# Performance work log

Hardware: AMD Instinct MI355X
Metric: run time of the kernel (lower is better)

## Reference

```python
import jax, jax.numpy as jnp
import numpy as np

NUM_EXPERTS = 8
TOP_K = 2
B, L, H = 4, 4096, 1024


def setup_inputs() -> dict:
    key = jax.random.key(0)
    ks = jax.random.split(key, 5)
    s = 1.0 / np.sqrt(H)
    return {
        "hidden_states": jax.random.normal(ks[0], (B, L, H), dtype=jnp.float32),
        "gate_w": jax.random.normal(ks[1], (H, NUM_EXPERTS), dtype=jnp.float32) * s,
        "w1": jax.random.normal(ks[2], (NUM_EXPERTS, H, 2 * H), dtype=jnp.float32) * s,
        "b1": jnp.zeros((NUM_EXPERTS, 2 * H), dtype=jnp.float32),
        "w2": jax.random.normal(ks[3], (NUM_EXPERTS, 2 * H, H), dtype=jnp.float32) * (1.0 / np.sqrt(2 * H)),
        "b2": jnp.zeros((NUM_EXPERTS, H), dtype=jnp.float32),
    }


def reference(hidden_states, gate_w, w1, b1, w2, b2):
    b, l, h = hidden_states.shape
    flat = hidden_states.reshape(-1, h)                      # [T, H]
    router_logits = flat @ gate_w                            # [T, E]
    probs = jax.nn.softmax(router_logits, axis=-1)
    weights, indices = jax.lax.top_k(probs, TOP_K)           # [T, K]
    weights = weights / jnp.sum(weights, axis=-1, keepdims=True)
    # combine[t, e] = sum_k weights[t, k] * 1{indices[t, k] == e}
    onehot = jax.nn.one_hot(indices, NUM_EXPERTS, dtype=flat.dtype)  # [T, K, E]
    combine = jnp.einsum('tk,tke->te', weights, onehot)      # [T, E]
    out = jnp.zeros_like(flat)
    for e in range(NUM_EXPERTS):  # fixed small expert loop; dense-compute, sparse-combine
        hdn = jax.nn.relu(flat @ w1[e] + b1[e])              # [T, 2H]
        y = hdn @ w2[e] + b2[e]                              # [T, H]
        out = out + combine[:, e:e + 1] * y
    return out.reshape(b, l, h)
```

## Files before the change

kernel.cpp:

```cpp
#include <hip/hip_runtime.h>
#include <hip/hip_bf16.h>
#include <stdint.h>

#define T_TOK 16384
#define HD    1024
#define HD2   2048
#define NE    8
#define ROWS  (2*T_TOK)
#define MAXT  264
#define MT256 136
#define RTOK  32

#define M_NT    256
#define M_OFFS  272
#define M_TILES 288

typedef __bf16 bf16x8 __attribute__((ext_vector_type(8)));
typedef float f32x4 __attribute__((ext_vector_type(4)));

#define GLD16(g, l) __builtin_amdgcn_global_load_lds( \
    (const __attribute__((address_space(1))) void*)(g), \
    (__attribute__((address_space(3))) void*)(l), 16, 0, 0)

__device__ inline unsigned short f2bf(float f) {
    unsigned int u = __float_as_uint(f);
    unsigned int r = (u + 0x7fffu + ((u >> 16) & 1u)) >> 16;
    return (unsigned short)r;
}

__global__ __launch_bounds__(256) void cvt_wT(const float* __restrict__ w,
                                              unsigned short* __restrict__ wt,
                                              int K, int N) {
    __shared__ float t[32][33];
    int e = blockIdx.z;
    int n0 = blockIdx.x * 32, k0 = blockIdx.y * 32;
    int r = threadIdx.x >> 3;
    int c4 = (threadIdx.x & 7) * 4;
    const float* src = w + ((size_t)e * K + k0 + r) * N + n0 + c4;
    float4 v = *(const float4*)src;
    t[r][c4] = v.x; t[r][c4+1] = v.y; t[r][c4+2] = v.z; t[r][c4+3] = v.w;
    __syncthreads();
    int cc = threadIdx.x & 7;
    ushort4 o;
    o.x = f2bf(t[cc*4+0][r]); o.y = f2bf(t[cc*4+1][r]);
    o.z = f2bf(t[cc*4+2][r]); o.w = f2bf(t[cc*4+3][r]);
    *(ushort4*)(wt + ((size_t)e * N + n0 + r) * K + k0 + cc*4) = o;
}

__global__ __launch_bounds__(256) void router_k(const float* __restrict__ x,
        const float* __restrict__ gw, int* __restrict__ meta,
        int* __restrict__ tok_e, int* __restrict__ tok_slot, float* __restrict__ tok_w,
        unsigned short* __restrict__ xb) {
    __shared__ float g[NE * HD];
    __shared__ int   le[RTOK * 2];
    __shared__ float lw[RTOK * 2];
    __shared__ int   lslot[RTOK * 2];
    __shared__ int   lcnt[NE];
    __shared__ int   lbase[NE];
    for (int i = threadIdx.x; i < NE * HD; i += 256) {
        int k = i >> 3, e = i & 7;
        g[e * HD + k] = gw[i];
    }
    if (threadIdx.x < NE) lcnt[threadIdx.x] = 0;
    __syncthreads();

    int wave = threadIdx.x >> 6, lane = threadIdx.x & 63;
    int t0 = blockIdx.x * RTOK;
    for (int i = 0; i < RTOK / 4; i++) {
        int tt = wave * (RTOK / 4) + i;
        int t = t0 + tt;
        const float4* xr = (const float4*)(x + (size_t)t * HD);
        float acc[NE];
#pragma unroll
        for (int e = 0; e < NE; e++) acc[e] = 0.f;
#pragma unroll
        for (int j = 0; j < HD / 256; j++) {
            float4 xv = xr[lane + 64 * j];
            ushort4 o4;
            o4.x = f2bf(xv.x); o4.y = f2bf(xv.y);
            o4.z = f2bf(xv.z); o4.w = f2bf(xv.w);
            *(ushort4*)(xb + (size_t)t * HD + (lane + 64 * j) * 4) = o4;
#pragma unroll
            for (int e = 0; e < NE; e++) {
                float4 gv = *(const float4*)&g[e * HD + (lane + 64 * j) * 4];
                acc[e] += xv.x * gv.x + xv.y * gv.y + xv.z * gv.z + xv.w * gv.w;
            }
        }
#pragma unroll
        for (int e = 0; e < NE; e++) {
            float v = acc[e];
#pragma unroll
            for (int off = 32; off > 0; off >>= 1) v += __shfl_down(v, off, 64);
            acc[e] = v;
        }
        if (lane == 0) {
            int e1 = 0; float l1 = acc[0];
#pragma unroll
            for (int e = 1; e < NE; e++) if (acc[e] > l1) { l1 = acc[e]; e1 = e; }
            int e2 = -1; float l2 = -3.0e38f;
#pragma unroll
            for (int e = 0; e < NE; e++) if (e != e1 && acc[e] > l2) { l2 = acc[e]; e2 = e; }
            float w1 = 1.f / (1.f + expf(l2 - l1));
            le[tt * 2] = e1;     le[tt * 2 + 1] = e2;
            lw[tt * 2] = w1;     lw[tt * 2 + 1] = 1.f - w1;
        }
    }
    __syncthreads();
    if (threadIdx.x < RTOK * 2)
        lslot[threadIdx.x] = atomicAdd(&lcnt[le[threadIdx.x]], 1);
    __syncthreads();
    if (threadIdx.x < NE)
        lbase[threadIdx.x] = atomicAdd(&meta[threadIdx.x * 32], lcnt[threadIdx.x]);
    __syncthreads();
    if (threadIdx.x < RTOK * 2) {
        int gi = t0 * 2 + threadIdx.x;
        int e = le[threadIdx.x];
        tok_e[gi]    = e;
        tok_slot[gi] = lbase[e] + lslot[threadIdx.x];
        tok_w[gi]    = lw[threadIdx.x];
    }
}

__global__ __launch_bounds__(64) void offsets_k(int* __restrict__ meta) {
    int lane = threadIdx.x;
    int cl = (lane < NE) ? meta[lane * 32] : 0;
    int cnt[NE], offs[NE], tbase[NE];
    int o = 0, tb = 0;
#pragma unroll
    for (int e = 0; e < NE; e++) {
        cnt[e] = __shfl(cl, e, 64);
        offs[e] = o;  o += cnt[e];
        tbase[e] = tb; tb += (cnt[e] + 255) >> 8;
    }
    int nt = tb;
    if (lane == 0) meta[M_NT] = nt;
    if (lane < NE) meta[M_OFFS + lane] = offs[lane];
    for (int i = lane; i < nt; i += 64) {
        int e = 0;
#pragma unroll
        for (int k = 1; k < NE; k++) if (i >= tbase[k]) e = k;
        int m = i - tbase[e];
        int r0 = offs[e] + m * 256;
        int re = offs[e] + cnt[e];
        if (r0 + 256 < re) re = r0 + 256;
        meta[M_TILES + i] = e;
        meta[M_TILES + MAXT + i] = r0;
        meta[M_TILES + 2 * MAXT + i] = re;
    }
}

__global__ __launch_bounds__(256) void scatter_k(const int* __restrict__ meta,
        const int* __restrict__ tok_e, const int* __restrict__ tok_slot,
        const float* __restrict__ tok_w, int* __restrict__ rows_tok,
        float* __restrict__ rows_w) {
    int i = blockIdx.x * 256 + threadIdx.x;
    const int* offs = meta + M_OFFS;
    int e = tok_e[i];
    int r = offs[e] + tok_slot[i];
    rows_tok[r] = i >> 1;
    rows_w[r] = tok_w[i];
}


#define ST_A(H, SB, KTN) do { \
    GLD16(pa[H][0] + (KTN) * 64, &As[(SB) + ((H) * 1024 + w * 64) * 8]); \
    GLD16(pa[H][1] + (KTN) * 64, &As[(SB) + ((H) * 1024 + 512 + w * 64) * 8]); } while (0)
#define ST_B(H, SB, KTN) do { \
    GLD16(pb[H][0] + (KTN) * 64, &Bs[(SB) + ((H) * 1024 + w * 64) * 8]); \
    GLD16(pb[H][1] + (KTN) * 64, &Bs[(SB) + ((H) * 1024 + 512 + w * 64) * 8]); } while (0)
#define LD_A(AH, RBUF) do { \
    _Pragma("unroll") \
    for (int im_ = 0; im_ < 4; im_++) { \
        int row_ = (AH) * 128 + wm * 64 + im_ * 16 + rl; \
        _Pragma("unroll") \
        for (int ks_ = 0; ks_ < 2; ks_++) { \
            int g_ = (ks_ * 4 + q) ^ (row_ & 7); \
            af[im_][ks_] = *(const bf16x8*)&As[(RBUF) + row_ * 64 + g_ * 8]; \
        } } } while (0)
#define LD_B(DST, BH, RBUF) do { \
    _Pragma("unroll") \
    for (int in_ = 0; in_ < 2; in_++) { \
        int row_ = (BH) * 128 + wn * 32 + in_ * 16 + rl; \
        _Pragma("unroll") \
        for (int ks_ = 0; ks_ < 2; ks_++) { \
            int g_ = (ks_ * 4 + q) ^ (row_ & 7); \
            DST[in_][ks_] = *(const bf16x8*)&Bs[(RBUF) + row_ * 64 + g_ * 8]; \
        } } } while (0)
#define MM(AH, BH, BF) do { \
    _Pragma("unroll") \
    for (int im_ = 0; im_ < 4; im_++) \
    _Pragma("unroll") \
    for (int in_ = 0; in_ < 2; in_++) \
    _Pragma("unroll") \
    for (int ks_ = 0; ks_ < 2; ks_++) \
        acc[AH][BH][im_][in_] = __builtin_amdgcn_mfma_f32_16x16x32_bf16( \
            af[im_][ks_], BF[in_][ks_], acc[AH][BH][im_][in_], 0, 0, 0); } while (0)
#define SB0()  __builtin_amdgcn_sched_barrier(0)
#define VMW4() do { asm volatile("s_waitcnt vmcnt(4)" ::: "memory"); SB0(); } while (0)
#define BAR()  do { __builtin_amdgcn_s_barrier(); SB0(); } while (0)
#define PRIO(P) __builtin_amdgcn_s_setprio(P)

__global__ __launch_bounds__(512, 2) void gemm1_k(
    const unsigned short* __restrict__ Xbf,
    const unsigned short* __restrict__ W1T,
    const float* __restrict__ b1,
    const int* __restrict__ meta,
    const int* __restrict__ rows_tok,
    unsigned short* __restrict__ hdn)
{
    __shared__ unsigned short As[2 * 16384];
    __shared__ unsigned short Bs[2 * 16384];
    int nt = meta[M_NT];
    int fid = blockIdx.y * 8 + blockIdx.x;
    int lid = (fid & 7) * MT256 + (fid >> 3);
    int xx = lid & 7, mt = lid >> 3;
    if (mt >= nt) return;
    int e    = meta[M_TILES + mt];
    int r0   = meta[M_TILES + MAXT + mt];
    int rend = meta[M_TILES + 2 * MAXT + mt];
    int n0 = xx * 256;

    int tid = threadIdx.x, w = tid >> 6, lane = tid & 63;
    int wm = w >> 2, wn = w & 3;
    int rl = lane & 15, q = lane >> 4;

    const unsigned short* pa[2][2];
    const unsigned short* pb[2][2];
#pragma unroll
    for (int h = 0; h < 2; h++)
#pragma unroll
        for (int c = 0; c < 2; c++) {
            int gg = c * 512 + tid;
            int row = gg >> 3, cc = gg & 7, cl = cc ^ (row & 7);
            int grow = r0 + h * 128 + row;
            grow = grow < ROWS - 1 ? grow : ROWS - 1;
            int tok = rows_tok[grow];
            pa[h][c] = Xbf + (size_t)tok * HD + cl * 8;
            pb[h][c] = W1T + ((size_t)e * HD2 + n0 + h * 128 + row) * HD + cl * 8;
        }

    f32x4 acc[2][2][4][2];
#pragma unroll
    for (int a = 0; a < 2; a++)
#pragma unroll
    for (int b = 0; b < 2; b++)
#pragma unroll
    for (int i = 0; i < 4; i++)
#pragma unroll
    for (int n = 0; n < 2; n++)
        acc[a][b][i][n] = (f32x4){0.f, 0.f, 0.f, 0.f};

    bf16x8 af[4][2], bf0[2][2], bf1[2][2];

    ST_A(0, 0, 0); ST_B(0, 0, 0); ST_B(1, 0, 0); ST_A(1, 0, 0);
    VMW4(); BAR();

#pragma unroll 1
    for (int kt = 0; kt < HD / 64; kt++) {
        int rbuf = (kt & 1) << 14;
        int sbuf = rbuf ^ 16384;
        int ktn = (kt + 1 < HD / 64) ? kt + 1 : HD / 64 - 1;
        LD_A(0, rbuf); LD_B(bf0, 0, rbuf);
        ST_A(0, sbuf, ktn);
        VMW4(); BAR();
        PRIO(1); MM(0, 0, bf0); PRIO(0);
        BAR();
        LD_B(bf1, 1, rbuf);
        ST_B(0, sbuf, ktn);
        VMW4(); BAR();
        PRIO(1); MM(0, 1, bf1); PRIO(0);
        BAR();
        LD_A(1, rbuf);
        ST_B(1, sbuf, ktn);
        BAR();
        PRIO(1); MM(1, 1, bf1); PRIO(0);
        BAR();
        LD_B(bf0, 0, rbuf);
        ST_A(1, sbuf, ktn);
        VMW4(); BAR();
        PRIO(1); MM(1, 0, bf0); PRIO(0);
        BAR();
    }

    const float* b1e = b1 + (size_t)e * HD2;
#pragma unroll
    for (int ah = 0; ah < 2; ah++)
#pragma unroll
    for (int bh = 0; bh < 2; bh++)
#pragma unroll
    for (int in = 0; in < 2; in++) {
        int col = n0 + bh * 128 + wn * 32 + in * 16 + rl;
        float bias = b1e[col];
#pragma unroll
        for (int im = 0; im < 4; im++) {
            int rb2 = r0 + ah * 128 + wm * 64 + im * 16 + q * 4;
#pragma unroll
            for (int j = 0; j < 4; j++) {
                int r = rb2 + j;
                if (r < rend) {
                    float v = acc[ah][bh][im][in][j] + bias;
                    v = v > 0.f ? v : 0.f;
                    hdn[(size_t)r * HD2 + col] = f2bf(v);
                }
            }
        }
    }
}

__global__ __launch_bounds__(512, 2) void gemm2_k(
    const unsigned short* __restrict__ hdn,
    const unsigned short* __restrict__ W2T,
    const float* __restrict__ b2,
    const int* __restrict__ meta,
    const int* __restrict__ rows_tok,
    const float* __restrict__ rows_w,
    float* __restrict__ out)
{
    __shared__ unsigned short As[2 * 16384];
    __shared__ unsigned short Bs[2 * 16384];
    int nt = meta[M_NT];
    int fid = blockIdx.y * 4 + blockIdx.x;
    int lid = (fid & 7) * (MT256 / 2) + (fid >> 3);
    int xx = lid & 3, mt = lid >> 2;
    if (mt >= nt) return;
    int e    = meta[M_TILES + mt];
    int r0   = meta[M_TILES + MAXT + mt];
    int rend = meta[M_TILES + 2 * MAXT + mt];
    int n0 = xx * 256;

    int tid = threadIdx.x, w = tid >> 6, lane = tid & 63;
    int wm = w >> 2, wn = w & 3;
    int rl = lane & 15, q = lane >> 4;

    const unsigned short* pa[2][2];
    const unsigned short* pb[2][2];
#pragma unroll
    for (int h = 0; h < 2; h++)
#pragma unroll
        for (int c = 0; c < 2; c++) {
            int gg = c * 512 + tid;
            int row = gg >> 3, cc = gg & 7, cl = cc ^ (row & 7);
            int grow = r0 + h * 128 + row;
            grow = grow < ROWS - 1 ? grow : ROWS - 1;
            pa[h][c] = hdn + (size_t)grow * HD2 + cl * 8;
            pb[h][c] = W2T + ((size_t)e * HD + n0 + h * 128 + row) * HD2 + cl * 8;
        }

    f32x4 acc[2][2][4][2];
#pragma unroll
    for (int a = 0; a < 2; a++)
#pragma unroll
    for (int b = 0; b < 2; b++)
#pragma unroll
    for (int i = 0; i < 4; i++)
#pragma unroll
    for (int n = 0; n < 2; n++)
        acc[a][b][i][n] = (f32x4){0.f, 0.f, 0.f, 0.f};

    bf16x8 af[4][2], bf0[2][2], bf1[2][2];

    ST_A(0, 0, 0); ST_B(0, 0, 0); ST_B(1, 0, 0); ST_A(1, 0, 0);
    VMW4(); BAR();

#pragma unroll 1
    for (int kt = 0; kt < HD2 / 64; kt++) {
        int rbuf = (kt & 1) << 14;
        int sbuf = rbuf ^ 16384;
        int ktn = (kt + 1 < HD2 / 64) ? kt + 1 : HD2 / 64 - 1;
        LD_A(0, rbuf); LD_B(bf0, 0, rbuf);
        ST_A(0, sbuf, ktn);
        VMW4(); BAR();
        PRIO(1); MM(0, 0, bf0); PRIO(0);
        BAR();
        LD_B(bf1, 1, rbuf);
        ST_B(0, sbuf, ktn);
        VMW4(); BAR();
        PRIO(1); MM(0, 1, bf1); PRIO(0);
        BAR();
        LD_A(1, rbuf);
        ST_B(1, sbuf, ktn);
        BAR();
        PRIO(1); MM(1, 1, bf1); PRIO(0);
        BAR();
        LD_B(bf0, 0, rbuf);
        ST_A(1, sbuf, ktn);
        VMW4(); BAR();
        PRIO(1); MM(1, 0, bf0); PRIO(0);
        BAR();
    }

    const float* b2e = b2 + (size_t)e * HD;
    float bias[2][2];
#pragma unroll
    for (int bh = 0; bh < 2; bh++)
#pragma unroll
        for (int in = 0; in < 2; in++)
            bias[bh][in] = b2e[n0 + bh * 128 + wn * 32 + in * 16 + rl];
#pragma unroll
    for (int ah = 0; ah < 2; ah++)
#pragma unroll
    for (int im = 0; im < 4; im++) {
        int rb2 = r0 + ah * 128 + wm * 64 + im * 16 + q * 4;
#pragma unroll
        for (int j = 0; j < 4; j++) {
            int r = rb2 + j;
            if (r < rend) {
                int tok = rows_tok[r];
                float wt = rows_w[r];
                float* op = out + (size_t)tok * HD + n0;
#pragma unroll
                for (int bh = 0; bh < 2; bh++)
#pragma unroll
                for (int in = 0; in < 2; in++) {
                    float v = (acc[ah][bh][im][in][j] + bias[bh][in]) * wt;
                    atomicAdd(op + bh * 128 + wn * 32 + in * 16 + rl, v);
                }
            }
        }
    }
}

extern "C" void kernel_launch(void* const* d_in, const int* in_sizes, int n_in,
                              void* d_out, int out_size, void* d_ws, size_t ws_size,
                              hipStream_t stream) {
    const float* x  = (const float*)d_in[0];
    const float* gw = (const float*)d_in[1];
    const float* w1 = (const float*)d_in[2];
    const float* b1 = (const float*)d_in[3];
    const float* w2 = (const float*)d_in[4];
    const float* b2 = (const float*)d_in[5];
    float* out = (float*)d_out;

    uint8_t* ws = (uint8_t*)d_ws;
    unsigned short* Xbf = (unsigned short*)(ws);
    unsigned short* W1T = (unsigned short*)(ws + 33554432ull);
    unsigned short* W2T = (unsigned short*)(ws + 67108864ull);
    unsigned short* HDN = (unsigned short*)(ws + 100663296ull);
    int*   meta     = (int*)(ws + 234881024ull);
    int*   tok_e    = meta + 2048;
    int*   tok_slot = tok_e + ROWS;
    float* tok_w    = (float*)(tok_slot + ROWS);
    int*   rows_tok = (int*)(tok_w + ROWS);
    float* rows_w   = (float*)(rows_tok + ROWS);

    hipMemsetAsync(meta, 0, 1024, stream);
    hipMemsetAsync(d_out, 0, (size_t)out_size * sizeof(float), stream);

    cvt_wT<<<dim3(HD2 / 32, HD / 32, NE), 256, 0, stream>>>(w1, W1T, HD, HD2);
    cvt_wT<<<dim3(HD / 32, HD2 / 32, NE), 256, 0, stream>>>(w2, W2T, HD2, HD);
    router_k<<<T_TOK / RTOK, 256, 0, stream>>>(x, gw, meta, tok_e, tok_slot, tok_w, Xbf);
    offsets_k<<<1, 64, 0, stream>>>(meta);
    scatter_k<<<ROWS / 256, 256, 0, stream>>>(meta, tok_e, tok_slot, tok_w, rows_tok, rows_w);
    gemm1_k<<<dim3(HD2 / 256, MT256), 512, 0, stream>>>(Xbf, W1T, b1, meta, rows_tok, HDN);
    gemm2_k<<<dim3(HD / 256, MT256), 512, 0, stream>>>(HDN, W2T, b2, meta, rows_tok, rows_w, out);
}
```

Before: 794.7 us.

## Replace double-buffered K=64 pipeline with 4-stage K=32 async load ring

Both expert GEMM kernels switch from a two-buffer K=64 tile loop, with four barrier-separated quarter-MMA phases and priority toggles, to a four-slot ring of K=32 tiles. Loads are issued three steps ahead and waited on with vmcnt(12). Each K step loads B fragments once and runs all A halves against them, with a new XOR swizzle for 32-wide LDS rows. The intent is deeper memory latency hiding and fewer barriers per unit of MFMA work. In exchange there are twice as many outer iterations with two barriers each, and the smaller K chunk per step may reduce load efficiency.

After: 756.5 us. 1.05x faster.

```diff
diff --git a/kernel.cpp b/kernel.cpp
--- a/kernel.cpp
+++ b/kernel.cpp
@@ -162,43 +162,45 @@
 }
 
 
-#define ST_A(H, SB, KTN) do { \
-    GLD16(pa[H][0] + (KTN) * 64, &As[(SB) + ((H) * 1024 + w * 64) * 8]); \
-    GLD16(pa[H][1] + (KTN) * 64, &As[(SB) + ((H) * 1024 + 512 + w * 64) * 8]); } while (0)
-#define ST_B(H, SB, KTN) do { \
-    GLD16(pb[H][0] + (KTN) * 64, &Bs[(SB) + ((H) * 1024 + w * 64) * 8]); \
-    GLD16(pb[H][1] + (KTN) * 64, &Bs[(SB) + ((H) * 1024 + 512 + w * 64) * 8]); } while (0)
-#define LD_A(AH, RBUF) do { \
+#define ISSUE(KK, NT_) do { \
+    int kk_ = (KK) < (NT_) ? (KK) : (NT_) - 1; \
+    int bb_ = ((KK) & 3) * 8192; \
+    GLD16(pa0 + kk_ * 32, &As[bb_ + (w * 64) * 8]); \
+    GLD16(pa1 + kk_ * 32, &As[bb_ + (512 + w * 64) * 8]); \
+    GLD16(pb0 + kk_ * 32, &Bs[bb_ + (w * 64) * 8]); \
+    GLD16(pb1 + kk_ * 32, &Bs[bb_ + (512 + w * 64) * 8]); } while (0)
+#define SB0()   __builtin_amdgcn_sched_barrier(0)
+#define VMW12() do { asm volatile("s_waitcnt vmcnt(12)" ::: "memory"); SB0(); } while (0)
+#define VMW0()  do { asm volatile("s_waitcnt vmcnt(0)" ::: "memory"); SB0(); } while (0)
+#define BAR()   do { __builtin_amdgcn_s_barrier(); SB0(); } while (0)
+
+#define KSTEP(RB) do { \
+    bf16x8 af[4], bfr[2][2]; \
     _Pragma("unroll") \
-    for (int im_ = 0; im_ < 4; im_++) { \
-        int row_ = (AH) * 128 + wm * 64 + im_ * 16 + rl; \
-        _Pragma("unroll") \
-        for (int ks_ = 0; ks_ < 2; ks_++) { \
-            int g_ = (ks_ * 4 + q) ^ (row_ & 7); \
-            af[im_][ks_] = *(const bf16x8*)&As[(RBUF) + row_ * 64 + g_ * 8]; \
-        } } } while (0)
-#define LD_B(DST, BH, RBUF) do { \
+    for (int bh_ = 0; bh_ < 2; bh_++) \
     _Pragma("unroll") \
     for (int in_ = 0; in_ < 2; in_++) { \
-        int row_ = (BH) * 128 + wn * 32 + in_ * 16 + rl; \
+        int row_ = bh_ * 128 + wn * 32 + in_ * 16 + rl; \
+        int ph_ = q ^ ((row_ >> 1) & 3); \
+        bfr[bh_][in_] = *(const bf16x8*)&Bs[(RB) + row_ * 32 + ph_ * 8]; \
+    } \
+    _Pragma("unroll") \
+    for (int ah_ = 0; ah_ < 2; ah_++) { \
         _Pragma("unroll") \
-        for (int ks_ = 0; ks_ < 2; ks_++) { \
-            int g_ = (ks_ * 4 + q) ^ (row_ & 7); \
-            DST[in_][ks_] = *(const bf16x8*)&Bs[(RBUF) + row_ * 64 + g_ * 8]; \
-        } } } while (0)
-#define MM(AH, BH, BF) do { \
-    _Pragma("unroll") \
-    for (int im_ = 0; im_ < 4; im_++) \
-    _Pragma("unroll") \
-    for (int in_ = 0; in_ < 2; in_++) \
-    _Pragma("unroll") \
-    for (int ks_ = 0; ks_ < 2; ks_++) \
-        acc[AH][BH][im_][in_] = __builtin_amdgcn_mfma_f32_16x16x32_bf16( \
-            af[im_][ks_], BF[in_][ks_], acc[AH][BH][im_][in_], 0, 0, 0); } while (0)
-#define SB0()  __builtin_amdgcn_sched_barrier(0)
-#define VMW4() do { asm volatile("s_waitcnt vmcnt(4)" ::: "memory"); SB0(); } while (0)
-#define BAR()  do { __builtin_amdgcn_s_barrier(); SB0(); } while (0)
-#define PRIO(P) __builtin_amdgcn_s_setprio(P)
+        for (int im_ = 0; im_ < 4; im_++) { \
+            int row_ = ah_ * 128 + wm * 64 + im_ * 16 + rl; \
+            int ph_ = q ^ ((row_ >> 1) & 3); \
+            af[im_] = *(const bf16x8*)&As[(RB) + row_ * 32 + ph_ * 8]; \
+        } \
+        _Pragma("unroll") \
+        for (int im_ = 0; im_ < 4; im_++) \
+        _Pragma("unroll") \
+        for (int bh_ = 0; bh_ < 2; bh_++) \
+        _Pragma("unroll") \
+        for (int in_ = 0; in_ < 2; in_++) \
+            acc[ah_][bh_][im_][in_] = __builtin_amdgcn_mfma_f32_16x16x32_bf16( \
+                af[im_], bfr[bh_][in_], acc[ah_][bh_][im_][in_], 0, 0, 0); \
+    } } while (0)
 
 __global__ __launch_bounds__(512, 2) void gemm1_k(
     const unsigned short* __restrict__ Xbf,
@@ -208,8 +210,8 @@
     const int* __restrict__ rows_tok,
     unsigned short* __restrict__ hdn)
 {
-    __shared__ unsigned short As[2 * 16384];
-    __shared__ unsigned short Bs[2 * 16384];
+    __shared__ unsigned short As[4 * 8192];
+    __shared__ unsigned short Bs[4 * 8192];
     int nt = meta[M_NT];
     int fid = blockIdx.y * 8 + blockIdx.x;
     int lid = (fid & 7) * MT256 + (fid >> 3);
@@ -224,20 +226,17 @@
     int wm = w >> 2, wn = w & 3;
     int rl = lane & 15, q = lane >> 4;
 
-    const unsigned short* pa[2][2];
-    const unsigned short* pb[2][2];
-#pragma unroll
-    for (int h = 0; h < 2; h++)
-#pragma unroll
-        for (int c = 0; c < 2; c++) {
-            int gg = c * 512 + tid;
-            int row = gg >> 3, cc = gg & 7, cl = cc ^ (row & 7);
-            int grow = r0 + h * 128 + row;
-            grow = grow < ROWS - 1 ? grow : ROWS - 1;
-            int tok = rows_tok[grow];
-            pa[h][c] = Xbf + (size_t)tok * HD + cl * 8;
-            pb[h][c] = W1T + ((size_t)e * HD2 + n0 + h * 128 + row) * HD + cl * 8;
-        }
+    const unsigned short *pa0, *pa1, *pb0, *pb1;
+    {
+        int gg = tid, row = gg >> 2, lc = (gg & 3) ^ ((row >> 1) & 3);
+        int grow = r0 + row; grow = grow < ROWS - 1 ? grow : ROWS - 1;
+        pa0 = Xbf + (size_t)rows_tok[grow] * HD + lc * 8;
+        pb0 = W1T + ((size_t)e * HD2 + n0 + row) * HD + lc * 8;
+        gg = 512 + tid; row = gg >> 2; lc = (gg & 3) ^ ((row >> 1) & 3);
+        grow = r0 + row; grow = grow < ROWS - 1 ? grow : ROWS - 1;
+        pa1 = Xbf + (size_t)rows_tok[grow] * HD + lc * 8;
+        pb1 = W1T + ((size_t)e * HD2 + n0 + row) * HD + lc * 8;
+    }
 
     f32x4 acc[2][2][4][2];
 #pragma unroll
@@ -250,37 +249,18 @@
     for (int n = 0; n < 2; n++)
         acc[a][b][i][n] = (f32x4){0.f, 0.f, 0.f, 0.f};
 
-    bf16x8 af[4][2], bf0[2][2], bf1[2][2];
-
-    ST_A(0, 0, 0); ST_B(0, 0, 0); ST_B(1, 0, 0); ST_A(1, 0, 0);
-    VMW4(); BAR();
-
-#pragma unroll 1
-    for (int kt = 0; kt < HD / 64; kt++) {
-        int rbuf = (kt & 1) << 14;
-        int sbuf = rbuf ^ 16384;
-        int ktn = (kt + 1 < HD / 64) ? kt + 1 : HD / 64 - 1;
-        LD_A(0, rbuf); LD_B(bf0, 0, rbuf);
-        ST_A(0, sbuf, ktn);
-        VMW4(); BAR();
-        PRIO(1); MM(0, 0, bf0); PRIO(0);
+    ISSUE(0, HD / 32); ISSUE(1, HD / 32); ISSUE(2, HD / 32);
+
+#pragma unroll 4
+    for (int kt = 0; kt < HD / 32; kt++) {
+        ISSUE(kt + 3, HD / 32);
+        SB0();
+        VMW12();
         BAR();
-        LD_B(bf1, 1, rbuf);
-        ST_B(0, sbuf, ktn);
-        VMW4(); BAR();
-        PRIO(1); MM(0, 1, bf1); PRIO(0);
+        KSTEP((kt & 3) * 8192);
         BAR();
-        LD_A(1, rbuf);
-        ST_B(1, sbuf, ktn);
-        BAR();
-        PRIO(1); MM(1, 1, bf1); PRIO(0);
-        BAR();
-        LD_B(bf0, 0, rbuf);
-        ST_A(1, sbuf, ktn);
-        VMW4(); BAR();
-        PRIO(1); MM(1, 0, bf0); PRIO(0);
-        BAR();
-    }
+    }
+    VMW0();
 
     const float* b1e = b1 + (size_t)e * HD2;
 #pragma unroll
@@ -316,8 +296,8 @@
     const float* __restrict__ rows_w,
     float* __restrict__ out)
 {
-    __shared__ unsigned short As[2 * 16384];
-    __shared__ unsigned short Bs[2 * 16384];
+    __shared__ unsigned short As[4 * 8192];
+    __shared__ unsigned short Bs[4 * 8192];
     int nt = meta[M_NT];
     int fid = blockIdx.y * 4 + blockIdx.x;
     int lid = (fid & 7) * (MT256 / 2) + (fid >> 3);
@@ -332,19 +312,17 @@
     int wm = w >> 2, wn = w & 3;
     int rl = lane & 15, q = lane >> 4;
 
-    const unsigned short* pa[2][2];
-    const unsigned short* pb[2][2];
-#pragma unroll
-    for (int h = 0; h < 2; h++)
-#pragma unroll
-        for (int c = 0; c < 2; c++) {
-            int gg = c * 512 + tid;
-            int row = gg >> 3, cc = gg & 7, cl = cc ^ (row & 7);
-            int grow = r0 + h * 128 + row;
-            grow = grow < ROWS - 1 ? grow : ROWS - 1;
-            pa[h][c] = hdn + (size_t)grow * HD2 + cl * 8;
-            pb[h][c] = W2T + ((size_t)e * HD + n0 + h * 128 + row) * HD2 + cl * 8;
-        }
+    const unsigned short *pa0, *pa1, *pb0, *pb1;
+    {
+        int gg = tid, row = gg >> 2, lc = (gg & 3) ^ ((row >> 1) & 3);
+        int grow = r0 + row; grow = grow < ROWS - 1 ? grow : ROWS - 1;
+        pa0 = hdn + (size_t)grow * HD2 + lc * 8;
+        pb0 = W2T + ((size_t)e * HD + n0 + row) * HD2 + lc * 8;
+        gg = 512 + tid; row = gg >> 2; lc = (gg & 3) ^ ((row >> 1) & 3);
+        grow = r0 + row; grow = grow < ROWS - 1 ? grow : ROWS - 1;
+        pa1 = hdn + (size_t)grow * HD2 + lc * 8;
+        pb1 = W2T + ((size_t)e * HD + n0 + row) * HD2 + lc * 8;
+    }
 
     f32x4 acc[2][2][4][2];
 #pragma unroll
@@ -357,37 +335,18 @@
     for (int n = 0; n < 2; n++)
         acc[a][b][i][n] = (f32x4){0.f, 0.f, 0.f, 0.f};
 
-    bf16x8 af[4][2], bf0[2][2], bf1[2][2];
-
-    ST_A(0, 0, 0); ST_B(0, 0, 0); ST_B(1, 0, 0); ST_A(1, 0, 0);
-    VMW4(); BAR();
-
-#pragma unroll 1
-    for (int kt = 0; kt < HD2 / 64; kt++) {
-        int rbuf = (kt & 1) << 14;
-        int sbuf = rbuf ^ 16384;
-        int ktn = (kt + 1 < HD2 / 64) ? kt + 1 : HD2 / 64 - 1;
-        LD_A(0, rbuf); LD_B(bf0, 0, rbuf);
-        ST_A(0, sbuf, ktn);
-        VMW4(); BAR();
-        PRIO(1); MM(0, 0, bf0); PRIO(0);
+    ISSUE(0, HD2 / 32); ISSUE(1, HD2 / 32); ISSUE(2, HD2 / 32);
+
+#pragma unroll 4
+    for (int kt = 0; kt < HD2 / 32; kt++) {
+        ISSUE(kt + 3, HD2 / 32);
+        SB0();
+        VMW12();
         BAR();
-        LD_B(bf1, 1, rbuf);
-        ST_B(0, sbuf, ktn);
-        VMW4(); BAR();
-        PRIO(1); MM(0, 1, bf1); PRIO(0);
+        KSTEP((kt & 3) * 8192);
         BAR();
-        LD_A(1, rbuf);
-        ST_B(1, sbuf, ktn);
-        BAR();
-        PRIO(1); MM(1, 1, bf1); PRIO(0);
-        BAR();
-        LD_B(bf0, 0, rbuf);
-        ST_A(1, sbuf, ktn);
-        VMW4(); BAR();
-        PRIO(1); MM(1, 0, bf0); PRIO(0);
-        BAR();
-    }
+    }
+    VMW0();
 
     const float* b2e = b2 + (size_t)e * HD;
     float bias[2][2];
```
